# Kernel optimization log

Measured on AMD Instinct MI355X. Metric: run time of the kernel, lower is better.

## Reference

```python
import jax, jax.numpy as jnp
import numpy as np

D_MODEL = 1024
N_HEADS = 16
D_FF = 4096
EPS = 1e-5


def _linear_init(key, fan_in, fan_out):
    # torch nn.Linear default: U(-1/sqrt(fan_in), 1/sqrt(fan_in))
    k1, k2 = jax.random.split(key)
    bound = 1.0 / np.sqrt(fan_in)
    W = jax.random.uniform(k1, (fan_in, fan_out), minval=-bound, maxval=bound, dtype=jnp.float32)
    b = jax.random.uniform(k2, (fan_out,), minval=-bound, maxval=bound, dtype=jnp.float32)
    return W, b


def setup_inputs() -> dict:
    key = jax.random.key(0)
    ks = jax.random.split(key, 8)
    x = jax.random.normal(ks[0], (4, 2048, D_MODEL), dtype=jnp.float32)
    Wq, bq = _linear_init(ks[1], D_MODEL, D_MODEL)
    Wk, bk = _linear_init(ks[2], D_MODEL, D_MODEL)
    Wv, bv = _linear_init(ks[3], D_MODEL, D_MODEL)
    Wo, bo = _linear_init(ks[4], D_MODEL, D_MODEL)
    W1, b1 = _linear_init(ks[5], D_MODEL, D_FF)
    W2, b2 = _linear_init(ks[6], D_FF, D_MODEL)
    g1 = jnp.ones((D_MODEL,), jnp.float32); be1 = jnp.zeros((D_MODEL,), jnp.float32)
    g2 = jnp.ones((D_MODEL,), jnp.float32); be2 = jnp.zeros((D_MODEL,), jnp.float32)
    return {"x": x, "Wq": Wq, "bq": bq, "Wk": Wk, "bk": bk, "Wv": Wv, "bv": bv,
            "Wo": Wo, "bo": bo, "g1": g1, "be1": be1, "W1": W1, "b1": b1,
            "W2": W2, "b2": b2, "g2": g2, "be2": be2}


def _layernorm(x, g, b):
    mu = jnp.mean(x, axis=-1, keepdims=True)
    var = jnp.mean(jnp.square(x - mu), axis=-1, keepdims=True)
    return (x - mu) * jax.lax.rsqrt(var + EPS) * g + b


def reference(x, Wq, bq, Wk, bk, Wv, bv, Wo, bo, g1, be1, W1, b1, W2, b2, g2, be2):
    B, T, D = x.shape
    H, dk = N_HEADS, D // N_HEADS
    # projections -> [B, H, T, dk]
    def split_heads(y):
        return y.reshape(B, T, H, dk).transpose(0, 2, 1, 3)
    Q = split_heads(x @ Wq + bq)
    K = split_heads(x @ Wk + bk)
    V = split_heads(x @ Wv + bv)
    scores = jnp.einsum('bhtd,bhsd->bhts', Q, K) / jnp.sqrt(jnp.float32(dk))
    weights = jax.nn.softmax(scores, axis=-1)  # no causal mask in original
    ctx = jnp.einsum('bhts,bhsd->bhtd', weights, V)
    ctx = ctx.transpose(0, 2, 1, 3).reshape(B, T, D)
    attn_out = ctx @ Wo + bo
    x = _layernorm(x + attn_out, g1, be1)
    ff = jax.nn.relu(x @ W1 + b1) @ W2 + b2
    x = _layernorm(x + ff, g2, be2)
    return x
```

## Files before the change

### kernel.cpp

```cpp
#include <hip/hip_runtime.h>
#include <hip/hip_bf16.h>
#include <stdint.h>

typedef __attribute__((ext_vector_type(8))) short short8;
typedef __attribute__((ext_vector_type(4))) float f32x4;
typedef __attribute__((ext_vector_type(16))) float f32x16;

#define SEQ 2048
#define DMODEL 1024
#define NH 16
#define DKH 64

__device__ __forceinline__ uint16_t f2b(float f) {
  uint32_t u = __float_as_uint(f);
  uint32_t r = (u + 0x7fff + ((u >> 16) & 1)) >> 16;
  return (uint16_t)r;
}
__device__ __forceinline__ float b2f(uint16_t u) {
  return __uint_as_float(((uint32_t)u) << 16);
}

__device__ __forceinline__ void gload16(const uint16_t* g, uint16_t* l) {
  __builtin_amdgcn_global_load_lds((const __attribute__((address_space(1))) void*)g,
                                   (__attribute__((address_space(3))) void*)l, 16, 0, 0);
}

__global__ __launch_bounds__(256) void k_castx(const float* __restrict__ x,
                                               uint16_t* __restrict__ xb) {
  int i = blockIdx.x * 256 + threadIdx.x;
  float4 v = reinterpret_cast<const float4*>(x)[i];
  uint16_t o[4] = {f2b(v.x), f2b(v.y), f2b(v.z), f2b(v.w)};
  reinterpret_cast<uint2*>(xb)[i] = *reinterpret_cast<uint2*>(o);
}

__global__ __launch_bounds__(256) void k_tcast_all(
    const float* __restrict__ Wq, const float* __restrict__ Wk, const float* __restrict__ Wv,
    const float* __restrict__ Wo, const float* __restrict__ W1, const float* __restrict__ W2,
    uint16_t* __restrict__ wt_qkv, uint16_t* __restrict__ wt_o, uint16_t* __restrict__ wt_1,
    uint16_t* __restrict__ wt_2) {
  __shared__ float tile[32][33];
  const int id = blockIdx.x;
  const float* W;
  uint16_t* Wt;
  int K, N, bx, by;
  if (id < 4096) {
    int wsel = id >> 10, r = id & 1023;
    K = 1024; N = 1024; bx = r & 31; by = r >> 5;
    W = wsel == 0 ? Wq : (wsel == 1 ? Wk : (wsel == 2 ? Wv : Wo));
    Wt = wsel == 3 ? wt_o : wt_qkv + wsel * 1024 * 1024;
  } else if (id < 8192) {
    int r = id - 4096;
    K = 1024; N = 4096; bx = r & 127; by = r >> 7;
    W = W1; Wt = wt_1;
  } else {
    int r = id - 8192;
    K = 4096; N = 1024; bx = r & 31; by = r >> 5;
    W = W2; Wt = wt_2;
  }
  const int n0 = bx * 32, k0 = by * 32;
  const int tx = threadIdx.x & 31, ty = threadIdx.x >> 5;
#pragma unroll
  for (int i = 0; i < 32; i += 8)
    tile[ty + i][tx] = W[(size_t)(k0 + ty + i) * N + n0 + tx];
  __syncthreads();
#pragma unroll
  for (int i = 0; i < 32; i += 8)
    Wt[(size_t)(n0 + ty + i) * K + k0 + tx] = f2b(tile[tx][ty + i]);
}

__global__ __launch_bounds__(256) void k_vtrans(const uint16_t* __restrict__ V,
                                                uint16_t* __restrict__ Vt) {
  __shared__ uint16_t tile[64][72];
  const int s0 = blockIdx.x * 64;
  const uint16_t* Vp = V + (size_t)blockIdx.y * SEQ * DKH;
  uint16_t* Vtp = Vt + (size_t)blockIdx.y * SEQ * DKH;
  const int t = threadIdx.x;
#pragma unroll
  for (int i = t; i < 512; i += 256) {
    int r = i >> 3, c8 = (i & 7) << 3;
    *reinterpret_cast<uint4*>(&tile[r][c8]) =
        *reinterpret_cast<const uint4*>(Vp + (size_t)(s0 + r) * DKH + c8);
  }
  __syncthreads();
#pragma unroll
  for (int i = t; i < 512; i += 256) {
    int d = i >> 3, s8 = (i & 7) << 3;
    uint16_t tmp[8];
#pragma unroll
    for (int j = 0; j < 8; ++j) tmp[j] = tile[s8 + j][d];
    *reinterpret_cast<uint4*>(Vtp + (size_t)d * SEQ + s0 + s8) = *reinterpret_cast<uint4*>(tmp);
  }
}

#define MODE_QKV 0
#define MODE_RAW 1
#define MODE_RELU 2

template <int BN, int MODE>
__global__ __launch_bounds__(512, 2) void k_gemm2(
    const uint16_t* __restrict__ A, const uint16_t* __restrict__ Bt, int M, int N, int K,
    int nx, const float* __restrict__ bias0, const float* __restrict__ bias1,
    const float* __restrict__ bias2, uint16_t* __restrict__ ob0, uint16_t* __restrict__ ob1,
    uint16_t* __restrict__ ob2, float* __restrict__ of) {
  constexpr int ASZ = 256 * 64;
  constexpr int BSZ = BN * 64;
  __shared__ __align__(16) uint16_t lds[2 * (ASZ + BSZ)];
  uint16_t* const Abase = lds;
  uint16_t* const Bbase = lds + 2 * ASZ;
  constexpr int WN = (BN == 256) ? 4 : 2;
  constexpr int MREP = (BN == 256) ? 8 : 4;
  constexpr int NPH = (BN == 256) ? 4 : 2;
  const int o = blockIdx.x;
  const int chunk = gridDim.x >> 3;
  const int wg = (o & 7) * chunk + (o >> 3);
  const int brow = (wg / nx) << 8;
  const int bcol = (wg % nx) * BN;
  const int t = threadIdx.x;
  const int wid = t >> 6, l = t & 63, g = l >> 4, lr = l & 15;
  const int wr = wid / WN, wc = wid % WN;
  const int wrow = wr * (MREP * 16);
  const int wcol = wc * 64;

  const int srow = t >> 3;
  const int ss0 = (t & 7) ^ (srow & 7);
  const int ss1 = (t & 7) ^ ((srow + 64) & 7);

  auto stage_half = [&](const uint16_t* gsrc, int grow0, int kk, uint16_t* ldst) {
    gload16(gsrc + (size_t)(grow0 + srow) * K + kk + ss0 * 8, ldst + t * 8);
    gload16(gsrc + (size_t)(grow0 + srow + 64) * K + kk + ss1 * 8, ldst + 4096 + t * 8);
  };
  auto rdfrag = [&](const uint16_t* buf, int ar, int kk) -> short8 {
    int slot = ((kk << 2) + g) ^ (ar & 7);
    return *reinterpret_cast<const short8*>(buf + ar * 64 + slot * 8);
  };

  f32x4 acc[MREP][4] = {};
  const int nt = K >> 6;

  stage_half(A, brow, 0, Abase);
  stage_half(A, brow + 128, 0, Abase + 8192);
  stage_half(Bt, bcol, 0, Bbase);
  if (BN == 256) stage_half(Bt, bcol + 128, 0, Bbase + 8192);
  __syncthreads();

  for (int kt = 0; kt < nt; ++kt) {
    const int cur = kt & 1;
    const uint16_t* Ac = Abase + cur * ASZ;
    const uint16_t* Bc = Bbase + cur * BSZ;
    uint16_t* An = Abase + (cur ^ 1) * ASZ;
    uint16_t* Bn = Bbase + (cur ^ 1) * BSZ;
    const bool pf = (kt + 1 < nt);
    const int knx = (kt + 1) << 6;
#pragma unroll
    for (int q = 0; q < NPH; ++q) {
      const int mq = (BN == 256) ? (q >> 1) : 0;
      const int nq = (BN == 256) ? (q & 1) : q;
      short8 af[4][2], bf[2][2];
#pragma unroll
      for (int j = 0; j < 4; ++j)
#pragma unroll
        for (int kk = 0; kk < 2; ++kk)
          af[j][kk] = rdfrag(Ac, wrow + (mq * 4 + j) * 16 + lr, kk);
#pragma unroll
      for (int j = 0; j < 2; ++j)
#pragma unroll
        for (int kk = 0; kk < 2; ++kk)
          bf[j][kk] = rdfrag(Bc, wcol + (nq * 2 + j) * 16 + lr, kk);
      if (pf) {
        if (q == 0) {
          stage_half(A, brow, knx, An);
          stage_half(A, brow + 128, knx, An + 8192);
          if (BN == 128) stage_half(Bt, bcol, knx, Bn);
        }
        if (BN == 256 && q == 1) stage_half(Bt, bcol, knx, Bn);
        if (BN == 256 && q == 2) stage_half(Bt, bcol + 128, knx, Bn + 8192);
      }
      __builtin_amdgcn_s_barrier();
      __builtin_amdgcn_s_setprio(1);
#pragma unroll
      for (int j = 0; j < 4; ++j)
#pragma unroll
        for (int j2 = 0; j2 < 2; ++j2)
#pragma unroll
          for (int kk = 0; kk < 2; ++kk)
            acc[mq * 4 + j][nq * 2 + j2] = __builtin_amdgcn_mfma_f32_16x16x32_bf16(
                af[j][kk], bf[j2][kk], acc[mq * 4 + j][nq * 2 + j2], 0, 0, 0);
      __builtin_amdgcn_s_setprio(0);
      if (q == NPH - 1) {
        asm volatile("s_waitcnt vmcnt(0)" ::: "memory");
        __builtin_amdgcn_s_barrier();
        __builtin_amdgcn_sched_barrier(0);
      } else {
        __builtin_amdgcn_s_barrier();
      }
    }
  }

#pragma unroll
  for (int m = 0; m < MREP; ++m) {
#pragma unroll
    for (int n = 0; n < 4; ++n) {
#pragma unroll
      for (int qi = 0; qi < 4; ++qi) {
        int r = brow + wrow + m * 16 + g * 4 + qi;
        int c = bcol + wcol + n * 16 + lr;
        float v = acc[m][n][qi];
        if (MODE == MODE_QKV) {
          int which = c >> 10;
          int hd = c & 1023;
          const float* bp = which == 0 ? bias0 : (which == 1 ? bias1 : bias2);
          v += bp[hd];
          if (which == 0) v *= 0.1803368801f;
          uint16_t* dst = which == 0 ? ob0 : (which == 1 ? ob1 : ob2);
          int b = r >> 11, tt = r & 2047;
          int h = hd >> 6, d = hd & 63;
          dst[((size_t)((b * NH + h) * SEQ + tt)) * DKH + d] = f2b(v);
        } else if (MODE == MODE_RELU) {
          v += bias0[c];
          v = fmaxf(v, 0.0f);
          ob0[(size_t)r * N + c] = f2b(v);
        } else {
          of[(size_t)r * N + c] = v;
        }
      }
    }
  }
}

__global__ __launch_bounds__(256) void k_attn(const uint16_t* __restrict__ Qb,
                                              const uint16_t* __restrict__ Kb,
                                              const uint16_t* __restrict__ Vtg,
                                              uint16_t* __restrict__ ctx) {
  __shared__ __align__(16) uint16_t Ks[2][64 * 64];
  __shared__ __align__(16) uint16_t Vs[2][64 * 64];
  __shared__ float l_arr[4][32];
  const int o = blockIdx.x;
  const int wg = (o & 7) * 128 + (o >> 3);
  const int qt = wg & 15;
  const int bh = wg >> 4;
  const int b = bh >> 4, h = bh & 15;
  const uint16_t* Qp = Qb + (size_t)bh * SEQ * DKH;
  const uint16_t* Kp = Kb + (size_t)bh * SEQ * DKH;
  const uint16_t* Vp = Vtg + (size_t)bh * SEQ * DKH;
  const int t = threadIdx.x, w = t >> 6, l = t & 63;
  const int lo5 = l & 31, hh = l >> 5;
  const int qbase = qt * 128 + w * 32;

  short8 qf[4];
#pragma unroll
  for (int kc = 0; kc < 4; ++kc)
    qf[kc] = *reinterpret_cast<const short8*>(Qp + (size_t)(qbase + lo5) * DKH + kc * 16 + hh * 8);

  f32x16 oacc[2] = {};
  float lsum = 0.f;

  const int swz = ((l & 7) ^ ((l >> 3) & 7)) << 3;
  const int ci0 = w * 2, ci1 = w * 2 + 1;
  const int r0 = ci0 * 8 + (l >> 3), r1 = ci1 * 8 + (l >> 3);
  uint16_t* ldsK0 = &Ks[0][0] + ci0 * 512 + l * 8;
  uint16_t* ldsK1 = &Ks[0][0] + ci1 * 512 + l * 8;
  uint16_t* ldsV0 = &Vs[0][0] + ci0 * 512 + l * 8;
  uint16_t* ldsV1 = &Vs[0][0] + ci1 * 512 + l * 8;
  const uint16_t* gK0 = Kp + (size_t)r0 * DKH + swz;
  const uint16_t* gK1 = Kp + (size_t)r1 * DKH + swz;
  const uint16_t* gV0 = Vp + (size_t)r0 * SEQ + swz;
  const uint16_t* gV1 = Vp + (size_t)r1 * SEQ + swz;

  gload16(gK0, ldsK0);
  gload16(gK1, ldsK1);
  gload16(gV0, ldsV0);
  gload16(gV1, ldsV1);
  __syncthreads();

  for (int tile = 0; tile < 32; ++tile) {
    const int cur = tile & 1;
    if (tile < 31) {
      const int nxt = (cur ^ 1) * 4096;
      const size_t s0n = (size_t)(tile + 1) * 64;
      gload16(gK0 + s0n * DKH, ldsK0 + nxt);
      gload16(gK1 + s0n * DKH, ldsK1 + nxt);
      gload16(gV0 + s0n, ldsV0 + nxt);
      gload16(gV1 + s0n, ldsV1 + nxt);
    }
    const char* Kbuf = reinterpret_cast<const char*>(&Ks[cur][0]);
    const char* Vbuf = reinterpret_cast<const char*>(&Vs[cur][0]);

#pragma unroll
    for (int sblk = 0; sblk < 2; ++sblk) {
      short8 kf[4];
      const int krow = sblk * 32 + lo5;
      const int kxor = (krow & 7) << 4;
#pragma unroll
      for (int kc = 0; kc < 4; ++kc) {
        int cb = (kc * 32 + hh * 16) ^ kxor;
        kf[kc] = *reinterpret_cast<const short8*>(Kbuf + krow * 128 + cb);
      }
      short8 vf[2][2];
#pragma unroll
      for (int scl = 0; scl < 2; ++scl)
#pragma unroll
        for (int dblk = 0; dblk < 2; ++dblk) {
          int vrow = dblk * 32 + lo5;
          int cb = (sblk * 64 + scl * 32 + hh * 16) ^ ((vrow & 7) << 4);
          vf[scl][dblk] = *reinterpret_cast<const short8*>(Vbuf + vrow * 128 + cb);
        }

      f32x16 sa = {};
      __builtin_amdgcn_s_setprio(1);
#pragma unroll
      for (int kc = 0; kc < 4; ++kc)
        sa = __builtin_amdgcn_mfma_f32_32x32x16_bf16(kf[kc], qf[kc], sa, 0, 0, 0);
      __builtin_amdgcn_s_setprio(0);

      float p[16];
      float ls = 0.f;
#pragma unroll
      for (int r = 0; r < 16; ++r) {
        p[r] = __builtin_amdgcn_exp2f(sa[r]);
        ls += p[r];
      }
      lsum += ls;

      uint32_t clo[4], chi[4];
#pragma unroll
      for (int m = 0; m < 4; ++m) {
        asm("v_cvt_pk_bf16_f32 %0, %1, %2" : "=v"(clo[m]) : "v"(p[4 * m]), "v"(p[4 * m + 1]));
        asm("v_cvt_pk_bf16_f32 %0, %1, %2" : "=v"(chi[m]) : "v"(p[4 * m + 2]), "v"(p[4 * m + 3]));
      }

#pragma unroll
      for (int scl = 0; scl < 2; ++scl) {
        uint32_t a0 = clo[2 * scl], b0 = clo[2 * scl + 1];
        uint32_t a1 = chi[2 * scl], b1 = chi[2 * scl + 1];
        asm("v_permlane32_swap_b32 %0, %1" : "+v"(a0), "+v"(b0));
        asm("v_permlane32_swap_b32 %0, %1" : "+v"(a1), "+v"(b1));
        union {
          uint32_t u[4];
          short8 s;
        } pu;
        pu.u[0] = a0;
        pu.u[1] = a1;
        pu.u[2] = b0;
        pu.u[3] = b1;
        __builtin_amdgcn_s_setprio(1);
#pragma unroll
        for (int dblk = 0; dblk < 2; ++dblk)
          oacc[dblk] = __builtin_amdgcn_mfma_f32_32x32x16_bf16(pu.s, vf[scl][dblk], oacc[dblk], 0, 0, 0);
        __builtin_amdgcn_s_setprio(0);
      }
    }
    __syncthreads();
  }

  {
    float full = lsum + __shfl_xor(lsum, 32, 64);
    if (l < 32) l_arr[w][lo5] = full;
  }
#pragma unroll
  for (int r = 0; r < 16; ++r) {
    int q = (r & 3) + 8 * (r >> 2) + 4 * hh;
    float li = 1.0f / l_arr[w][q];
    int rowg = b * SEQ + qbase + q;
#pragma unroll
    for (int dblk = 0; dblk < 2; ++dblk) {
      int colg = h * DKH + dblk * 32 + lo5;
      ctx[(size_t)rowg * DMODEL + colg] = f2b(oacc[dblk][r] * li);
    }
  }
}

template <bool WRITE_B, bool RESBF>
__global__ __launch_bounds__(256) void k_ln(const float* __restrict__ in,
                                            const float* __restrict__ bias,
                                            const void* __restrict__ res,
                                            const float* __restrict__ gam,
                                            const float* __restrict__ bet,
                                            float* __restrict__ outf,
                                            uint16_t* __restrict__ outb) {
  const int row = blockIdx.x;
  const int t = threadIdx.x, lane = t & 63, w = t >> 6;
  float4 v = reinterpret_cast<const float4*>(in + (size_t)row * DMODEL)[t];
  float4 bb0 = reinterpret_cast<const float4*>(bias)[t];
  float4 rr;
  if (RESBF) {
    uint2 ru = reinterpret_cast<const uint2*>((const uint16_t*)res + (size_t)row * DMODEL)[t];
    const uint16_t* rp = reinterpret_cast<const uint16_t*>(&ru);
    rr.x = b2f(rp[0]);
    rr.y = b2f(rp[1]);
    rr.z = b2f(rp[2]);
    rr.w = b2f(rp[3]);
  } else {
    rr = reinterpret_cast<const float4*>((const float*)res + (size_t)row * DMODEL)[t];
  }
  v.x += bb0.x + rr.x;
  v.y += bb0.y + rr.y;
  v.z += bb0.z + rr.z;
  v.w += bb0.w + rr.w;
  float s = v.x + v.y + v.z + v.w;
  float s2 = v.x * v.x + v.y * v.y + v.z * v.z + v.w * v.w;
#pragma unroll
  for (int off = 1; off < 64; off <<= 1) {
    s += __shfl_xor(s, off, 64);
    s2 += __shfl_xor(s2, off, 64);
  }
  __shared__ float rs[4], rq[4];
  if (lane == 0) {
    rs[w] = s;
    rq[w] = s2;
  }
  __syncthreads();
  float ts = rs[0] + rs[1] + rs[2] + rs[3];
  float tq = rq[0] + rq[1] + rq[2] + rq[3];
  const float inv = 1.0f / DMODEL;
  float mu = ts * inv;
  float var = tq * inv - mu * mu;
  float rstd = rsqrtf(var + 1e-5f);
  float4 gg = reinterpret_cast<const float4*>(gam)[t];
  float4 bb = reinterpret_cast<const float4*>(bet)[t];
  float4 y;
  y.x = (v.x - mu) * rstd * gg.x + bb.x;
  y.y = (v.y - mu) * rstd * gg.y + bb.y;
  y.z = (v.z - mu) * rstd * gg.z + bb.z;
  y.w = (v.w - mu) * rstd * gg.w + bb.w;
  if (WRITE_B) {
    uint16_t oo[4] = {f2b(y.x), f2b(y.y), f2b(y.z), f2b(y.w)};
    reinterpret_cast<uint2*>(outb)[(size_t)row * 256 + t] = *reinterpret_cast<uint2*>(oo);
  } else {
    reinterpret_cast<float4*>(outf)[(size_t)row * 256 + t] = y;
  }
}

extern "C" void kernel_launch(void* const* d_in, const int* in_sizes, int n_in, void* d_out,
                              int out_size, void* d_ws, size_t ws_size, hipStream_t stream) {
  const float* x = (const float*)d_in[0];
  const float* Wq = (const float*)d_in[1];
  const float* bq = (const float*)d_in[2];
  const float* Wk = (const float*)d_in[3];
  const float* bk = (const float*)d_in[4];
  const float* Wv = (const float*)d_in[5];
  const float* bv = (const float*)d_in[6];
  const float* Wo = (const float*)d_in[7];
  const float* bo = (const float*)d_in[8];
  const float* g1 = (const float*)d_in[9];
  const float* be1 = (const float*)d_in[10];
  const float* W1 = (const float*)d_in[11];
  const float* b1 = (const float*)d_in[12];
  const float* W2 = (const float*)d_in[13];
  const float* b2 = (const float*)d_in[14];
  const float* g2 = (const float*)d_in[15];
  const float* be2 = (const float*)d_in[16];

  char* ws = (char*)d_ws;
  size_t off = 0;
  auto alloc = [&](size_t bytes) {
    char* p = ws + off;
    off += (bytes + 255) & ~(size_t)255;
    return p;
  };
  uint16_t* wt_qkv = (uint16_t*)alloc(3072ull * 1024 * 2);
  uint16_t* wt_o = (uint16_t*)alloc(1024ull * 1024 * 2);
  uint16_t* wt_1 = (uint16_t*)alloc(4096ull * 1024 * 2);
  uint16_t* wt_2 = (uint16_t*)alloc(1024ull * 4096 * 2);
  uint16_t* xb = (uint16_t*)alloc(8192ull * 1024 * 2);
  float* sum1 = (float*)alloc(8192ull * 1024 * 4);
  uint16_t* vt = (uint16_t*)alloc(8192ull * 1024 * 2);
  char* big = alloc(16777216ull + 67108864ull);
  uint16_t* Qbuf = (uint16_t*)big;
  uint16_t* Kbuf = (uint16_t*)(big + 16777216ull);
  uint16_t* Vbuf = (uint16_t*)(big + 2 * 16777216ull);
  uint16_t* ctx = xb;
  uint16_t* x1b = (uint16_t*)big;
  uint16_t* hbuf = (uint16_t*)(big + 16777216ull);
  (void)ws_size;

  k_tcast_all<<<12288, 256, 0, stream>>>(Wq, Wk, Wv, Wo, W1, W2, wt_qkv, wt_o, wt_1, wt_2);
  k_castx<<<8192, 256, 0, stream>>>(x, xb);
  k_gemm2<128, MODE_QKV><<<768, 512, 0, stream>>>(
      xb, wt_qkv, 8192, 3072, 1024, 24, bq, bk, bv, Qbuf, Kbuf, Vbuf, nullptr);
  k_vtrans<<<dim3(32, 64), 256, 0, stream>>>(Vbuf, vt);
  k_attn<<<1024, 256, 0, stream>>>(Qbuf, Kbuf, vt, ctx);
  k_gemm2<128, MODE_RAW><<<256, 512, 0, stream>>>(
      ctx, wt_o, 8192, 1024, 1024, 8, nullptr, nullptr, nullptr, nullptr, nullptr, nullptr, sum1);
  k_ln<true, false><<<8192, 256, 0, stream>>>(sum1, bo, x, g1, be1, nullptr, x1b);
  k_gemm2<256, MODE_RELU><<<512, 512, 0, stream>>>(
      x1b, wt_1, 8192, 4096, 1024, 16, b1, nullptr, nullptr, hbuf, nullptr, nullptr, nullptr);
  k_gemm2<128, MODE_RAW><<<256, 512, 0, stream>>>(
      hbuf, wt_2, 8192, 1024, 4096, 8, nullptr, nullptr, nullptr, nullptr, nullptr, nullptr, sum1);
  k_ln<false, true><<<8192, 256, 0, stream>>>(sum1, b2, x1b, g2, be2, (float*)d_out, nullptr);
}
```

Measured before the change: 401.9 us.

## Merge weight and input cast kernels, front-load GEMM prefetch, batch QK MFMAs

Combines the weight transpose-cast kernel and the input cast kernel into one launch, so one kernel launch and the gap between the two disappear. In the GEMM, all next-tile global-to-LDS staging is now issued in the first phase instead of being spread across phases. In attention, both QK score MFMA blocks are computed before the softmax and PV work, which gives more independent MFMA work to overlap. The cost is higher register pressure in attention and a burst of memory traffic at the start of each GEMM k-step.

```diff
diff --git a/kernel.cpp b/kernel.cpp
--- a/kernel.cpp
+++ b/kernel.cpp
@@ -25,21 +25,20 @@
                                    (__attribute__((address_space(3))) void*)l, 16, 0, 0);
 }
 
-__global__ __launch_bounds__(256) void k_castx(const float* __restrict__ x,
-                                               uint16_t* __restrict__ xb) {
-  int i = blockIdx.x * 256 + threadIdx.x;
-  float4 v = reinterpret_cast<const float4*>(x)[i];
-  uint16_t o[4] = {f2b(v.x), f2b(v.y), f2b(v.z), f2b(v.w)};
-  reinterpret_cast<uint2*>(xb)[i] = *reinterpret_cast<uint2*>(o);
-}
-
-__global__ __launch_bounds__(256) void k_tcast_all(
+__global__ __launch_bounds__(256) void k_prep(
     const float* __restrict__ Wq, const float* __restrict__ Wk, const float* __restrict__ Wv,
     const float* __restrict__ Wo, const float* __restrict__ W1, const float* __restrict__ W2,
-    uint16_t* __restrict__ wt_qkv, uint16_t* __restrict__ wt_o, uint16_t* __restrict__ wt_1,
-    uint16_t* __restrict__ wt_2) {
+    const float* __restrict__ x, uint16_t* __restrict__ wt_qkv, uint16_t* __restrict__ wt_o,
+    uint16_t* __restrict__ wt_1, uint16_t* __restrict__ wt_2, uint16_t* __restrict__ xb) {
+  const int id = blockIdx.x;
+  if (id >= 12288) {
+    int i = (id - 12288) * 256 + threadIdx.x;
+    float4 v = reinterpret_cast<const float4*>(x)[i];
+    uint16_t o[4] = {f2b(v.x), f2b(v.y), f2b(v.z), f2b(v.w)};
+    reinterpret_cast<uint2*>(xb)[i] = *reinterpret_cast<uint2*>(o);
+    return;
+  }
   __shared__ float tile[32][33];
-  const int id = blockIdx.x;
   const float* W;
   uint16_t* Wt;
   int K, N, bx, by;
@@ -166,14 +165,11 @@
 #pragma unroll
         for (int kk = 0; kk < 2; ++kk)
           bf[j][kk] = rdfrag(Bc, wcol + (nq * 2 + j) * 16 + lr, kk);
-      if (pf) {
-        if (q == 0) {
-          stage_half(A, brow, knx, An);
-          stage_half(A, brow + 128, knx, An + 8192);
-          if (BN == 128) stage_half(Bt, bcol, knx, Bn);
-        }
-        if (BN == 256 && q == 1) stage_half(Bt, bcol, knx, Bn);
-        if (BN == 256 && q == 2) stage_half(Bt, bcol + 128, knx, Bn + 8192);
+      if (pf && q == 0) {
+        stage_half(A, brow, knx, An);
+        stage_half(A, brow + 128, knx, An + 8192);
+        stage_half(Bt, bcol, knx, Bn);
+        if (BN == 256) stage_half(Bt, bcol + 128, knx, Bn + 8192);
       }
       __builtin_amdgcn_s_barrier();
       __builtin_amdgcn_s_setprio(1);
@@ -285,16 +281,31 @@
     const char* Kbuf = reinterpret_cast<const char*>(&Ks[cur][0]);
     const char* Vbuf = reinterpret_cast<const char*>(&Vs[cur][0]);
 
+    short8 kf[2][4];
 #pragma unroll
     for (int sblk = 0; sblk < 2; ++sblk) {
-      short8 kf[4];
       const int krow = sblk * 32 + lo5;
       const int kxor = (krow & 7) << 4;
 #pragma unroll
       for (int kc = 0; kc < 4; ++kc) {
         int cb = (kc * 32 + hh * 16) ^ kxor;
-        kf[kc] = *reinterpret_cast<const short8*>(Kbuf + krow * 128 + cb);
-      }
+        kf[sblk][kc] = *reinterpret_cast<const short8*>(Kbuf + krow * 128 + cb);
+      }
+    }
+    f32x16 sa[2];
+#pragma unroll
+    for (int sblk = 0; sblk < 2; ++sblk) {
+      f32x16 z = {};
+      __builtin_amdgcn_s_setprio(1);
+#pragma unroll
+      for (int kc = 0; kc < 4; ++kc)
+        z = __builtin_amdgcn_mfma_f32_32x32x16_bf16(kf[sblk][kc], qf[kc], z, 0, 0, 0);
+      __builtin_amdgcn_s_setprio(0);
+      sa[sblk] = z;
+    }
+
+#pragma unroll
+    for (int sblk = 0; sblk < 2; ++sblk) {
       short8 vf[2][2];
 #pragma unroll
       for (int scl = 0; scl < 2; ++scl)
@@ -305,18 +316,11 @@
           vf[scl][dblk] = *reinterpret_cast<const short8*>(Vbuf + vrow * 128 + cb);
         }
 
-      f32x16 sa = {};
-      __builtin_amdgcn_s_setprio(1);
-#pragma unroll
-      for (int kc = 0; kc < 4; ++kc)
-        sa = __builtin_amdgcn_mfma_f32_32x32x16_bf16(kf[kc], qf[kc], sa, 0, 0, 0);
-      __builtin_amdgcn_s_setprio(0);
-
       float p[16];
       float ls = 0.f;
 #pragma unroll
       for (int r = 0; r < 16; ++r) {
-        p[r] = __builtin_amdgcn_exp2f(sa[r]);
+        p[r] = __builtin_amdgcn_exp2f(sa[sblk][r]);
         ls += p[r];
       }
       lsum += ls;
@@ -473,8 +477,7 @@
   uint16_t* hbuf = (uint16_t*)(big + 16777216ull);
   (void)ws_size;
 
-  k_tcast_all<<<12288, 256, 0, stream>>>(Wq, Wk, Wv, Wo, W1, W2, wt_qkv, wt_o, wt_1, wt_2);
-  k_castx<<<8192, 256, 0, stream>>>(x, xb);
+  k_prep<<<20480, 256, 0, stream>>>(Wq, Wk, Wv, Wo, W1, W2, x, wt_qkv, wt_o, wt_1, wt_2, xb);
   k_gemm2<128, MODE_QKV><<<768, 512, 0, stream>>>(
       xb, wt_qkv, 8192, 3072, 1024, 24, bq, bk, bv, Qbuf, Kbuf, Vbuf, nullptr);
   k_vtrans<<<dim3(32, 64), 256, 0, stream>>>(Vbuf, vt);
```

Result: no change. 399.0 us (-0.7%).
